# Kernel optimization log

Hardware: AMD Instinct MI355X
Metric: run time of the kernel (lower is better)

Reference implementation:

```python
import jax, jax.numpy as jnp
import numpy as np

N, E, IN, HID, OUT, H, G = 50000, 800000, 128, 32, 32, 4, 64
NEG_SLOPE = 0.2


def setup_inputs() -> dict:
    key = jax.random.key(0)
    ks = jax.random.split(key, 12)
    p = lambda k, s: jax.random.normal(k, s, jnp.float32) * 0.1
    x = jax.random.normal(ks[0], (N, IN), jnp.float32)
    edge_index = jax.random.randint(ks[1], (2, E), 0, N, dtype=jnp.int64)
    batch = jnp.sort(jax.random.randint(ks[2], (N,), 0, G, dtype=jnp.int64))
    return {
        'x': x, 'edge_index': edge_index, 'batch': batch,
        'W1': p(ks[3], (IN, H * HID)),
        'att_src1': p(ks[4], (H, HID)), 'att_dst1': p(ks[5], (H, HID)),
        'b1': jnp.zeros((H * HID,), jnp.float32),
        'W2': p(ks[6], (H * HID, H * OUT)),
        'att_src2': p(ks[7], (H, OUT)), 'att_dst2': p(ks[8], (H, OUT)),
        'b2': jnp.zeros((H * OUT,), jnp.float32),
        'lin_w': p(ks[9], (H * OUT, 1)),
        'lin_b': jnp.zeros((1,), jnp.float32),
    }


def gat_conv(x, src, dst, W, a_src, a_dst, b, heads, ch):
    # x: [N, F_in]; src/dst: [E'] with self-loops already appended.
    n = x.shape[0]
    h = (x @ W).reshape(n, heads, ch)                      # [N, H, C]
    alpha_s = jnp.einsum('nhc,hc->nh', h, a_src)           # [N, H]
    alpha_d = jnp.einsum('nhc,hc->nh', h, a_dst)
    e = jax.nn.leaky_relu(alpha_s[src] + alpha_d[dst], NEG_SLOPE)  # [E', H]
    # segment softmax over destination neighborhoods
    m = jax.ops.segment_max(e, dst, num_segments=n)
    m = jnp.where(jnp.isfinite(m), m, 0.0)
    ex = jnp.exp(e - m[dst])
    s = jax.ops.segment_sum(ex, dst, num_segments=n)
    alpha = ex / (s[dst] + 1e-16)                          # [E', H]
    out = jax.ops.segment_sum(alpha[:, :, None] * h[src], dst, num_segments=n)
    return out.reshape(n, heads * ch) + b


def reference(x, edge_index, batch, W1, att_src1, att_dst1, b1,
              W2, att_src2, att_dst2, b2, lin_w, lin_b):
    # add self-loops (PyG GATConv default add_self_loops=True)
    loops = jnp.arange(N, dtype=edge_index.dtype)
    src = jnp.concatenate([edge_index[0], loops])
    dst = jnp.concatenate([edge_index[1], loops])

    h = jax.nn.elu(gat_conv(x, src, dst, W1, att_src1, att_dst1, b1, H, HID))
    h = gat_conv(h, src, dst, W2, att_src2, att_dst2, b2, H, OUT)  # [N, H*OUT]

    # global mean + max pool per graph
    counts = jax.ops.segment_sum(jnp.ones((N,), h.dtype), batch, num_segments=G)
    mean_p = jax.ops.segment_sum(h, batch, num_segments=G) / jnp.maximum(counts, 1.0)[:, None]
    max_p = jax.ops.segment_max(h, batch, num_segments=G)
    max_p = jnp.where(jnp.isfinite(max_p), max_p, 0.0)
    pooled = mean_p + max_p                                # [G, H*OUT]
    return pooled @ lin_w + lin_b                          # [G, 1]
```

## Files before the change

### kernel.cpp

```cpp
#include <hip/hip_runtime.h>
#include <hip/hip_bf16.h>
#include <hip/hip_fp16.h>
#include <math.h>

#define NEG_SLOPE 0.2f
#define BCAP 80

typedef _Float16 half8 __attribute__((ext_vector_type(8)));


__device__ __forceinline__ int lbound(const int* __restrict__ a, int n, int key) {
    int lo = 0, hi = n;
    while (lo < hi) {
        int mid = (lo + hi) >> 1;
        if (a[mid] < key) lo = mid + 1; else hi = mid;
    }
    return lo;
}

__device__ __forceinline__ unsigned encf(float f) {
    unsigned u = __float_as_uint(f);
    return (u & 0x80000000u) ? ~u : (u | 0x80000000u);
}
__device__ __forceinline__ float decf(unsigned u) {
    return (u & 0x80000000u) ? __uint_as_float(u & 0x7FFFFFFFu) : __uint_as_float(~u);
}


__global__ void init_kernel(int* __restrict__ cnt, int* __restrict__ col,
                            float* __restrict__ gsum, unsigned* __restrict__ gmax,
                            int n, int gtot) {
    int i = blockIdx.x * blockDim.x + threadIdx.x;
    if (i < n) {
        cnt[i] = 1;
        col[(size_t)i * BCAP] = i;
    }
    if (i < gtot) { gsum[i] = 0.f; gmax[i] = 0x007FFFFFu;  }
}

__global__ void build_kernel(const int* __restrict__ src, const int* __restrict__ dst,
                             int* __restrict__ cnt, int* __restrict__ col, int E) {
    int i = blockIdx.x * blockDim.x + threadIdx.x;
    if (i >= E) return;
    int d = dst[i];
    int slot = atomicAdd(&cnt[d], 1);
    if (slot < BCAP) col[(size_t)d * BCAP + slot] = src[i];
}


__global__ __launch_bounds__(256) void gemm_attn_kernel(
        const float* __restrict__ A, const float* __restrict__ W,
        const float* __restrict__ att_src, const float* __restrict__ att_dst,
        _Float16* __restrict__ H16, float* __restrict__ as_, float* __restrict__ ad_,
        int M) {
    __shared__ float xs[64][33];
    __shared__ float ws[32][132];

    int tid = threadIdx.x;
    int tr = tid >> 4;
    int tc = tid & 15;
    int m0 = blockIdx.x * 64;

    float acc[4][8];
    #pragma unroll
    for (int i = 0; i < 4; ++i)
        #pragma unroll
        for (int j = 0; j < 8; ++j) acc[i][j] = 0.f;

    for (int k0 = 0; k0 < 128; k0 += 32) {
        #pragma unroll
        for (int t = 0; t < 2; ++t) {
            int f = tid + t * 256;
            int r = f >> 3;
            int c4 = (f & 7) << 2;
            int gr = m0 + r; if (gr >= M) gr = M - 1;
            const float4 v = *(const float4*)(A + (size_t)gr * 128 + k0 + c4);
            xs[r][c4 + 0] = v.x; xs[r][c4 + 1] = v.y;
            xs[r][c4 + 2] = v.z; xs[r][c4 + 3] = v.w;
        }
        #pragma unroll
        for (int t = 0; t < 4; ++t) {
            int f = tid + t * 256;
            int r = f >> 5;
            int c4 = (f & 31) << 2;
            const float4 v = *(const float4*)(W + (size_t)(k0 + r) * 128 + c4);
            *(float4*)&ws[r][c4] = v;
        }
        __syncthreads();
        #pragma unroll
        for (int kk = 0; kk < 32; ++kk) {
            float a[4];
            #pragma unroll
            for (int i = 0; i < 4; ++i) a[i] = xs[4 * tr + i][kk];
            float4 b0 = *(const float4*)&ws[kk][8 * tc];
            float4 b1 = *(const float4*)&ws[kk][8 * tc + 4];
            float b[8] = { b0.x, b0.y, b0.z, b0.w, b1.x, b1.y, b1.z, b1.w };
            #pragma unroll
            for (int i = 0; i < 4; ++i)
                #pragma unroll
                for (int j = 0; j < 8; ++j)
                    acc[i][j] += a[i] * b[j];
        }
        __syncthreads();
    }

    const float4 s0 = *(const float4*)(att_src + 8 * tc);
    const float4 s1 = *(const float4*)(att_src + 8 * tc + 4);
    const float4 d0 = *(const float4*)(att_dst + 8 * tc);
    const float4 d1 = *(const float4*)(att_dst + 8 * tc + 4);
    int headw = tc >> 2;

    #pragma unroll
    for (int i = 0; i < 4; ++i) {
        int gr = m0 + 4 * tr + i;
        float psrc = acc[i][0]*s0.x + acc[i][1]*s0.y + acc[i][2]*s0.z + acc[i][3]*s0.w
                   + acc[i][4]*s1.x + acc[i][5]*s1.y + acc[i][6]*s1.z + acc[i][7]*s1.w;
        float pdst = acc[i][0]*d0.x + acc[i][1]*d0.y + acc[i][2]*d0.z + acc[i][3]*d0.w
                   + acc[i][4]*d1.x + acc[i][5]*d1.y + acc[i][6]*d1.z + acc[i][7]*d1.w;
        psrc += __shfl_xor(psrc, 1, 64); psrc += __shfl_xor(psrc, 2, 64);
        pdst += __shfl_xor(pdst, 1, 64); pdst += __shfl_xor(pdst, 2, 64);
        if (gr < M) {
            half8 hv;
            #pragma unroll
            for (int j = 0; j < 8; ++j) hv[j] = (_Float16)acc[i][j];
            *(half8*)(H16 + (size_t)gr * 128 + 8 * tc) = hv;
            if ((tc & 3) == 0) {
                as_[(size_t)gr * 4 + headw] = psrc;
                ad_[(size_t)gr * 4 + headw] = pdst;
            }
        }
    }
}


__global__ __launch_bounds__(256) void agg_kernel(
        const int* __restrict__ cnt, const int* __restrict__ col,
        const _Float16* __restrict__ h16, const float* __restrict__ as_,
        const float* __restrict__ ad_, const float* __restrict__ bias,
        float* __restrict__ out, int n, int elu) {
    __shared__ int   s_col[4][64];
    __shared__ float s_w[4][256];
    __shared__ int   s_nchunk;

    int wvb  = threadIdx.x >> 6;
    int lane = threadIdx.x & 63;
    int wv   = blockIdx.x * 4 + wvb;
    int valid = (wv < n);
    if (!valid) wv = n - 1;

    int deg = cnt[wv]; if (deg > BCAP) deg = BCAP;
    const int* crow = col + (size_t)wv * BCAP;
    const float4 adv = *(const float4*)(ad_ + (size_t)wv * 4);

    if (threadIdx.x == 0) s_nchunk = 0;
    __syncthreads();
    if (lane == 0) atomicMax(&s_nchunk, (deg + 63) >> 6);
    __syncthreads();
    int nchunk = s_nchunk;

    int q = lane >> 4;
    int r = lane & 15;
    int head = r >> 2;
    const _Float16* hrow = h16 + 8 * r;

    float l0 = 0.f, l1 = 0.f, l2 = 0.f, l3 = 0.f;
    float acc[8];
    #pragma unroll
    for (int j = 0; j < 8; ++j) acc[j] = 0.f;

    for (int c = 0; c < nchunk; ++c) {
        int c0 = c << 6;
        int cl = deg - c0;
        cl = cl < 0 ? 0 : (cl > 64 ? 64 : cl);
        if (lane < cl) {
            int s = crow[c0 + lane];
            const float4 av = *(const float4*)(as_ + (size_t)s * 4);
            float e0 = av.x + adv.x, e1 = av.y + adv.y;
            float e2 = av.z + adv.z, e3 = av.w + adv.w;
            float w0 = __expf(fmaxf(e0, NEG_SLOPE * e0));
            float w1 = __expf(fmaxf(e1, NEG_SLOPE * e1));
            float w2 = __expf(fmaxf(e2, NEG_SLOPE * e2));
            float w3 = __expf(fmaxf(e3, NEG_SLOPE * e3));
            l0 += w0; l1 += w1; l2 += w2; l3 += w3;
            s_col[wvb][lane] = s;
            *(float4*)&s_w[wvb][lane * 4] = make_float4(w0, w1, w2, w3);
        } else {
            s_col[wvb][lane] = 0;
            *(float4*)&s_w[wvb][lane * 4] = make_float4(0.f, 0.f, 0.f, 0.f);
        }
        __syncthreads();
        for (int it = 0; it < cl; it += 16) {
            int ea = it + q;
            int eb = ea + 4;
            int ec = ea + 8;
            int ed = ea + 12;
            int sa = s_col[wvb][ea];
            int sb = s_col[wvb][eb];
            int sc = s_col[wvb][ec];
            int sd = s_col[wvb][ed];
            float wa = s_w[wvb][ea * 4 + head];
            float wb = s_w[wvb][eb * 4 + head];
            float wc = s_w[wvb][ec * 4 + head];
            float wd = s_w[wvb][ed * 4 + head];
            const half8 ha = *(const half8*)(hrow + (size_t)sa * 128);
            const half8 hb = *(const half8*)(hrow + (size_t)sb * 128);
            const half8 hc = *(const half8*)(hrow + (size_t)sc * 128);
            const half8 hd = *(const half8*)(hrow + (size_t)sd * 128);
            #pragma unroll
            for (int j = 0; j < 8; ++j)
                acc[j] += wa * (float)ha[j] + wb * (float)hb[j]
                        + wc * (float)hc[j] + wd * (float)hd[j];
        }
        __syncthreads();
    }

    #pragma unroll
    for (int j = 0; j < 8; ++j) {
        acc[j] += __shfl_xor(acc[j], 16, 64);
        acc[j] += __shfl_xor(acc[j], 32, 64);
    }

    #pragma unroll
    for (int off = 1; off < 64; off <<= 1) {
        l0 += __shfl_xor(l0, off, 64);
        l1 += __shfl_xor(l1, off, 64);
        l2 += __shfl_xor(l2, off, 64);
        l3 += __shfl_xor(l3, off, 64);
    }

    if (lane < 16 && valid) {
        float lh = head == 0 ? l0 : head == 1 ? l1 : head == 2 ? l2 : l3;
        float inv = 1.f / (lh + 1e-16f);
        const float4 bv0 = *(const float4*)(bias + 8 * r);
        const float4 bv1 = *(const float4*)(bias + 8 * r + 4);
        float o[8];
        o[0] = acc[0] * inv + bv0.x; o[1] = acc[1] * inv + bv0.y;
        o[2] = acc[2] * inv + bv0.z; o[3] = acc[3] * inv + bv0.w;
        o[4] = acc[4] * inv + bv1.x; o[5] = acc[5] * inv + bv1.y;
        o[6] = acc[6] * inv + bv1.z; o[7] = acc[7] * inv + bv1.w;
        if (elu) {
            #pragma unroll
            for (int j = 0; j < 8; ++j) o[j] = o[j] > 0.f ? o[j] : expm1f(o[j]);
        }
        *(float4*)(out + (size_t)wv * 128 + 8 * r)     = make_float4(o[0], o[1], o[2], o[3]);
        *(float4*)(out + (size_t)wv * 128 + 8 * r + 4) = make_float4(o[4], o[5], o[6], o[7]);
    }
}


__global__ void pool1_kernel(const float* __restrict__ h, const int* __restrict__ batch,
                             float* __restrict__ gsum, unsigned* __restrict__ gmax, int n) {
    int g = blockIdx.x >> 3;
    int p = blockIdx.x & 7;
    int c = threadIdx.x;
    int s = lbound(batch, n, g);
    int e = lbound(batch, n, g + 1);
    int len = e - s;
    int lo = s + (int)((long long)len * p / 8);
    int hi = s + (int)((long long)len * (p + 1) / 8);
    float sum = 0.f, mx = -INFINITY;
    for (int i = lo; i < hi; ++i) {
        float v = h[(size_t)i * 128 + c];
        sum += v; mx = fmaxf(mx, v);
    }
    if (hi > lo) {
        atomicAdd(&gsum[g * 128 + c], sum);
        atomicMax(&gmax[g * 128 + c], encf(mx));
    }
}

__global__ void pool2_kernel(const float* __restrict__ gsum, const unsigned* __restrict__ gmax,
                             const int* __restrict__ batch, const float* __restrict__ lin_w,
                             const float* __restrict__ lin_b, float* __restrict__ out, int n) {
    int g = blockIdx.x;
    int c = threadIdx.x;
    int s = lbound(batch, n, g);
    int e = lbound(batch, n, g + 1);
    float cnt = fmaxf((float)(e - s), 1.0f);
    float mean = gsum[g * 128 + c] / cnt;
    float mx = decf(gmax[g * 128 + c]);
    if (!isfinite(mx)) mx = 0.f;
    float v = (mean + mx) * lin_w[c];
    __shared__ float red[128];
    red[c] = v;
    __syncthreads();
    for (int off = 64; off > 0; off >>= 1) {
        if (c < off) red[c] += red[c + off];
        __syncthreads();
    }
    if (c == 0) out[g] = red[0] + lin_b[0];
}


extern "C" void kernel_launch(void* const* d_in, const int* in_sizes, int n_in,
                              void* d_out, int out_size, void* d_ws, size_t ws_size,
                              hipStream_t stream) {
    const float* x    = (const float*)d_in[0];
    const int*   ei   = (const int*)d_in[1];
    const int*   batch= (const int*)d_in[2];
    const float* W1   = (const float*)d_in[3];
    const float* at_s1= (const float*)d_in[4];
    const float* at_d1= (const float*)d_in[5];
    const float* b1   = (const float*)d_in[6];
    const float* W2   = (const float*)d_in[7];
    const float* at_s2= (const float*)d_in[8];
    const float* at_d2= (const float*)d_in[9];
    const float* b2   = (const float*)d_in[10];
    const float* lw   = (const float*)d_in[11];
    const float* lb   = (const float*)d_in[12];
    float* out = (float*)d_out;

    const int N = in_sizes[0] / 128;
    const int E = in_sizes[1] / 2;
    const int G = out_size;

    char* p = (char*)d_ws;
    auto carve = [&](size_t bytes) -> void* {
        void* q = (void*)p;
        p += (bytes + 255) & ~(size_t)255;
        return q;
    };
    _Float16* h16    = (_Float16*)carve((size_t)N * 128 * 2);
    float*    agg    = (float*)carve((size_t)N * 128 * 4);
    float*    asb    = (float*)carve((size_t)N * 4 * 4);
    float*    adb    = (float*)carve((size_t)N * 4 * 4);
    int*      cnt    = (int*)carve((size_t)N * 4);
    int*      col    = (int*)carve((size_t)N * BCAP * 4);
    float*    gsum   = (float*)carve((size_t)G * 128 * 4);
    unsigned* gmax   = (unsigned*)carve((size_t)G * 128 * 4);

    const int* esrc = ei;
    const int* edst = ei + E;

    int initN = (N > G * 128) ? N : G * 128;
    init_kernel<<<(initN + 255) / 256, 256, 0, stream>>>(cnt, col, gsum, gmax, N, G * 128);
    build_kernel<<<(E + 255) / 256, 256, 0, stream>>>(esrc, edst, cnt, col, E);

    gemm_attn_kernel<<<(N + 63) / 64, 256, 0, stream>>>(x, W1, at_s1, at_d1, h16, asb, adb, N);
    agg_kernel<<<(N + 3) / 4, 256, 0, stream>>>(cnt, col, h16, asb, adb, b1, agg, N, 1);

    gemm_attn_kernel<<<(N + 63) / 64, 256, 0, stream>>>(agg, W2, at_s2, at_d2, h16, asb, adb, N);
    agg_kernel<<<(N + 3) / 4, 256, 0, stream>>>(cnt, col, h16, asb, adb, b2, agg, N, 0);

    pool1_kernel<<<G * 8, 128, 0, stream>>>(agg, batch, gsum, gmax, N);
    pool2_kernel<<<G, 128, 0, stream>>>(gsum, gmax, batch, lw, lb, out, N);
}
```

Baseline: 332.3 us.

## Use split-fp16 MFMA for GEMM and widen aggregation gather unroll

Replaces the FP32 scalar-FMA tiled GEMM with MFMA 16x16x32 f16 instructions. Both A and W are split into hi/lo fp16 parts to approximate fp32 accuracy using three MFMAs per tile. A new prep kernel repacks the weights into the MFMA operand layout. The aggregation loop also processes 8 neighbor gathers per step instead of 4 to expose more memory-level parallelism. This costs extra launches and register pressure, and the output stores in the epilogue become scalar fp16 writes.

```diff
diff --git a/kernel.cpp b/kernel.cpp
--- a/kernel.cpp
+++ b/kernel.cpp
@@ -5,8 +5,11 @@
 
 #define NEG_SLOPE 0.2f
 #define BCAP 80
+#define LAYER_W 16384
 
 typedef _Float16 half8 __attribute__((ext_vector_type(8)));
+typedef _Float16 half4v __attribute__((ext_vector_type(4)));
+typedef float f32x4 __attribute__((ext_vector_type(4)));
 
 
 __device__ __forceinline__ int lbound(const int* __restrict__ a, int n, int key) {
@@ -48,88 +51,114 @@
 }
 
 
+__global__ void wprep_kernel(const float* __restrict__ W1, const float* __restrict__ W2,
+                             _Float16* __restrict__ wt_hi, _Float16* __restrict__ wt_lo) {
+    int b = blockIdx.x;
+    int layer = b >> 5;
+    int nt = (b >> 2) & 7;
+    int kc = b & 3;
+    const float* W = layer ? W2 : W1;
+    int lane = threadIdx.x;
+    int n = lane & 15, q = lane >> 4;
+    size_t base = (size_t)layer * LAYER_W + (size_t)((nt * 4 + kc) * 64 + lane) * 8;
+    #pragma unroll
+    for (int j = 0; j < 8; ++j) {
+        int k = kc * 32 + q * 8 + j;
+        float w = W[(size_t)k * 128 + nt * 16 + n];
+        _Float16 hi = (_Float16)w;
+        wt_hi[base + j] = hi;
+        wt_lo[base + j] = (_Float16)(w - (float)hi);
+    }
+}
+
+
 __global__ __launch_bounds__(256) void gemm_attn_kernel(
-        const float* __restrict__ A, const float* __restrict__ W,
+        const float* __restrict__ A,
+        const _Float16* __restrict__ wt_hi, const _Float16* __restrict__ wt_lo,
         const float* __restrict__ att_src, const float* __restrict__ att_dst,
         _Float16* __restrict__ H16, float* __restrict__ as_, float* __restrict__ ad_,
         int M) {
-    __shared__ float xs[64][33];
-    __shared__ float ws[32][132];
+    __shared__ _Float16 a_hi[64][136];
+    __shared__ _Float16 a_lo[64][136];
 
     int tid = threadIdx.x;
-    int tr = tid >> 4;
-    int tc = tid & 15;
     int m0 = blockIdx.x * 64;
 
-    float acc[4][8];
-    #pragma unroll
-    for (int i = 0; i < 4; ++i)
+    #pragma unroll
+    for (int t = 0; t < 8; ++t) {
+        int f = tid + t * 256;
+        int r = f >> 5;
+        int c4 = (f & 31) << 2;
+        int gr = m0 + r; if (gr >= M) gr = M - 1;
+        const float4 v = *(const float4*)(A + (size_t)gr * 128 + c4);
+        _Float16 h0 = (_Float16)v.x, h1 = (_Float16)v.y;
+        _Float16 h2 = (_Float16)v.z, h3 = (_Float16)v.w;
+        half4v hi = { h0, h1, h2, h3 };
+        half4v lo = { (_Float16)(v.x - (float)h0), (_Float16)(v.y - (float)h1),
+                      (_Float16)(v.z - (float)h2), (_Float16)(v.w - (float)h3) };
+        *(half4v*)&a_hi[r][c4] = hi;
+        *(half4v*)&a_lo[r][c4] = lo;
+    }
+    __syncthreads();
+
+    int w = tid >> 6;
+    int lane = tid & 63;
+    int cbase = lane & 15;
+    int q = lane >> 4;
+    int mrow = (w << 4) + cbase;
+
+    f32x4 acc[8];
+    #pragma unroll
+    for (int nt = 0; nt < 8; ++nt) acc[nt] = (f32x4){0.f, 0.f, 0.f, 0.f};
+
+    #pragma unroll
+    for (int kc = 0; kc < 4; ++kc) {
+        half8 ah = *(half8*)&a_hi[mrow][kc * 32 + q * 8];
+        half8 al = *(half8*)&a_lo[mrow][kc * 32 + q * 8];
         #pragma unroll
-        for (int j = 0; j < 8; ++j) acc[i][j] = 0.f;
-
-    for (int k0 = 0; k0 < 128; k0 += 32) {
+        for (int nt = 0; nt < 8; ++nt) {
+            const half8 bh = *(const half8*)(wt_hi + (size_t)((nt * 4 + kc) * 64 + lane) * 8);
+            const half8 bl = *(const half8*)(wt_lo + (size_t)((nt * 4 + kc) * 64 + lane) * 8);
+            acc[nt] = __builtin_amdgcn_mfma_f32_16x16x32_f16(ah, bh, acc[nt], 0, 0, 0);
+            acc[nt] = __builtin_amdgcn_mfma_f32_16x16x32_f16(al, bh, acc[nt], 0, 0, 0);
+            acc[nt] = __builtin_amdgcn_mfma_f32_16x16x32_f16(ah, bl, acc[nt], 0, 0, 0);
+        }
+    }
+
+    float ps[4][4], pd[4][4];
+    #pragma unroll
+    for (int h = 0; h < 4; ++h)
         #pragma unroll
-        for (int t = 0; t < 2; ++t) {
-            int f = tid + t * 256;
-            int r = f >> 3;
-            int c4 = (f & 7) << 2;
-            int gr = m0 + r; if (gr >= M) gr = M - 1;
-            const float4 v = *(const float4*)(A + (size_t)gr * 128 + k0 + c4);
-            xs[r][c4 + 0] = v.x; xs[r][c4 + 1] = v.y;
-            xs[r][c4 + 2] = v.z; xs[r][c4 + 3] = v.w;
-        }
+        for (int i = 0; i < 4; ++i) { ps[h][i] = 0.f; pd[h][i] = 0.f; }
+
+    #pragma unroll
+    for (int nt = 0; nt < 8; ++nt) {
+        int c = nt * 16 + cbase;
+        float sv = att_src[c], dv = att_dst[c];
+        int h = nt >> 1;
         #pragma unroll
-        for (int t = 0; t < 4; ++t) {
-            int f = tid + t * 256;
-            int r = f >> 5;
-            int c4 = (f & 31) << 2;
-            const float4 v = *(const float4*)(W + (size_t)(k0 + r) * 128 + c4);
-            *(float4*)&ws[r][c4] = v;
-        }
-        __syncthreads();
+        for (int i = 0; i < 4; ++i) {
+            ps[h][i] += acc[nt][i] * sv;
+            pd[h][i] += acc[nt][i] * dv;
+            int gr = m0 + (w << 4) + (q << 2) + i;
+            if (gr < M) H16[(size_t)gr * 128 + c] = (_Float16)acc[nt][i];
+        }
+    }
+    #pragma unroll
+    for (int h = 0; h < 4; ++h)
         #pragma unroll
-        for (int kk = 0; kk < 32; ++kk) {
-            float a[4];
-            #pragma unroll
-            for (int i = 0; i < 4; ++i) a[i] = xs[4 * tr + i][kk];
-            float4 b0 = *(const float4*)&ws[kk][8 * tc];
-            float4 b1 = *(const float4*)&ws[kk][8 * tc + 4];
-            float b[8] = { b0.x, b0.y, b0.z, b0.w, b1.x, b1.y, b1.z, b1.w };
-            #pragma unroll
-            for (int i = 0; i < 4; ++i)
-                #pragma unroll
-                for (int j = 0; j < 8; ++j)
-                    acc[i][j] += a[i] * b[j];
-        }
-        __syncthreads();
-    }
-
-    const float4 s0 = *(const float4*)(att_src + 8 * tc);
-    const float4 s1 = *(const float4*)(att_src + 8 * tc + 4);
-    const float4 d0 = *(const float4*)(att_dst + 8 * tc);
-    const float4 d1 = *(const float4*)(att_dst + 8 * tc + 4);
-    int headw = tc >> 2;
-
-    #pragma unroll
-    for (int i = 0; i < 4; ++i) {
-        int gr = m0 + 4 * tr + i;
-        float psrc = acc[i][0]*s0.x + acc[i][1]*s0.y + acc[i][2]*s0.z + acc[i][3]*s0.w
-                   + acc[i][4]*s1.x + acc[i][5]*s1.y + acc[i][6]*s1.z + acc[i][7]*s1.w;
-        float pdst = acc[i][0]*d0.x + acc[i][1]*d0.y + acc[i][2]*d0.z + acc[i][3]*d0.w
-                   + acc[i][4]*d1.x + acc[i][5]*d1.y + acc[i][6]*d1.z + acc[i][7]*d1.w;
-        psrc += __shfl_xor(psrc, 1, 64); psrc += __shfl_xor(psrc, 2, 64);
-        pdst += __shfl_xor(pdst, 1, 64); pdst += __shfl_xor(pdst, 2, 64);
-        if (gr < M) {
-            half8 hv;
-            #pragma unroll
-            for (int j = 0; j < 8; ++j) hv[j] = (_Float16)acc[i][j];
-            *(half8*)(H16 + (size_t)gr * 128 + 8 * tc) = hv;
-            if ((tc & 3) == 0) {
-                as_[(size_t)gr * 4 + headw] = psrc;
-                ad_[(size_t)gr * 4 + headw] = pdst;
+        for (int i = 0; i < 4; ++i) {
+            float a = ps[h][i], b = pd[h][i];
+            #pragma unroll
+            for (int off = 1; off < 16; off <<= 1) {
+                a += __shfl_xor(a, off, 64);
+                b += __shfl_xor(b, off, 64);
             }
-        }
-    }
+            if (cbase == 0) {
+                int gr = m0 + (w << 4) + (q << 2) + i;
+                if (gr < M) { as_[(size_t)gr * 4 + h] = a; ad_[(size_t)gr * 4 + h] = b; }
+            }
+        }
 }
 
 
@@ -189,27 +218,25 @@
             *(float4*)&s_w[wvb][lane * 4] = make_float4(0.f, 0.f, 0.f, 0.f);
         }
         __syncthreads();
-        for (int it = 0; it < cl; it += 16) {
-            int ea = it + q;
-            int eb = ea + 4;
-            int ec = ea + 8;
-            int ed = ea + 12;
-            int sa = s_col[wvb][ea];
-            int sb = s_col[wvb][eb];
-            int sc = s_col[wvb][ec];
-            int sd = s_col[wvb][ed];
-            float wa = s_w[wvb][ea * 4 + head];
-            float wb = s_w[wvb][eb * 4 + head];
-            float wc = s_w[wvb][ec * 4 + head];
-            float wd = s_w[wvb][ed * 4 + head];
-            const half8 ha = *(const half8*)(hrow + (size_t)sa * 128);
-            const half8 hb = *(const half8*)(hrow + (size_t)sb * 128);
-            const half8 hc = *(const half8*)(hrow + (size_t)sc * 128);
-            const half8 hd = *(const half8*)(hrow + (size_t)sd * 128);
-            #pragma unroll
-            for (int j = 0; j < 8; ++j)
-                acc[j] += wa * (float)ha[j] + wb * (float)hb[j]
-                        + wc * (float)hc[j] + wd * (float)hd[j];
+        for (int it = 0; it < cl; it += 32) {
+            int ss[8]; float ww[8];
+            #pragma unroll
+            for (int u = 0; u < 8; ++u) {
+                int e = it + q + 4 * u;
+                ss[u] = s_col[wvb][e];
+                ww[u] = s_w[wvb][e * 4 + head];
+            }
+            half8 hh[8];
+            #pragma unroll
+            for (int u = 0; u < 8; ++u)
+                hh[u] = *(const half8*)(hrow + (size_t)ss[u] * 128);
+            #pragma unroll
+            for (int j = 0; j < 8; ++j) {
+                float v = 0.f;
+                #pragma unroll
+                for (int u = 0; u < 8; ++u) v += ww[u] * (float)hh[u][j];
+                acc[j] += v;
+            }
         }
         __syncthreads();
     }
@@ -328,6 +355,8 @@
     int*      col    = (int*)carve((size_t)N * BCAP * 4);
     float*    gsum   = (float*)carve((size_t)G * 128 * 4);
     unsigned* gmax   = (unsigned*)carve((size_t)G * 128 * 4);
+    _Float16* wt_hi  = (_Float16*)carve((size_t)2 * LAYER_W * 2);
+    _Float16* wt_lo  = (_Float16*)carve((size_t)2 * LAYER_W * 2);
 
     const int* esrc = ei;
     const int* edst = ei + E;
@@ -335,11 +364,14 @@
     int initN = (N > G * 128) ? N : G * 128;
     init_kernel<<<(initN + 255) / 256, 256, 0, stream>>>(cnt, col, gsum, gmax, N, G * 128);
     build_kernel<<<(E + 255) / 256, 256, 0, stream>>>(esrc, edst, cnt, col, E);
-
-    gemm_attn_kernel<<<(N + 63) / 64, 256, 0, stream>>>(x, W1, at_s1, at_d1, h16, asb, adb, N);
+    wprep_kernel<<<64, 64, 0, stream>>>(W1, W2, wt_hi, wt_lo);
+
+    gemm_attn_kernel<<<(N + 63) / 64, 256, 0, stream>>>(
+        x, wt_hi, wt_lo, at_s1, at_d1, h16, asb, adb, N);
     agg_kernel<<<(N + 3) / 4, 256, 0, stream>>>(cnt, col, h16, asb, adb, b1, agg, N, 1);
 
-    gemm_attn_kernel<<<(N + 63) / 64, 256, 0, stream>>>(agg, W2, at_s2, at_d2, h16, asb, adb, N);
+    gemm_attn_kernel<<<(N + 63) / 64, 256, 0, stream>>>(
+        agg, wt_hi + LAYER_W, wt_lo + LAYER_W, at_s2, at_d2, h16, asb, adb, N);
     agg_kernel<<<(N + 3) / 4, 256, 0, stream>>>(cnt, col, h16, asb, adb, b2, agg, N, 0);
 
     pool1_kernel<<<G * 8, 128, 0, stream>>>(agg, batch, gsum, gmax, N);
```

Result: slower. 342.9 us (+3.2%).
